# Kernel optimization log

Hardware: AMD Instinct MI355X
Metric: run time of the kernel (lower is better)

The kernel has to match this reference:

```python
import jax, jax.numpy as jnp
import numpy as np

B, T, D, H = 4, 2048, 1024, 16


def setup_inputs() -> dict:
    key = jax.random.key(0)
    ks = jax.random.split(key, 5)
    s = 0.02  # keep activations sane
    return {
        "x": jax.random.normal(ks[0], (B, T, D), jnp.float32),
        "Wq": jax.random.normal(ks[1], (D, D), jnp.float32) * s,
        "bq": jnp.zeros((D,), jnp.float32),
        "Wk": jax.random.normal(ks[2], (D, D), jnp.float32) * s,
        "bk": jnp.zeros((D,), jnp.float32),
        "Wv": jax.random.normal(ks[3], (D, D), jnp.float32) * s,
        "bv": jnp.zeros((D,), jnp.float32),
        "Wo": jax.random.normal(ks[4], (D, D), jnp.float32) * s,
        "bo": jnp.zeros((D,), jnp.float32),
    }


def _split_heads(t):  # (B,T,D) -> (B,H,T,d)
    b, s, d = t.shape
    return t.reshape(b, s, H, d // H).transpose(0, 2, 1, 3)


def reference(x, Wq, bq, Wk, bk, Wv, bv, Wo, bo):
    d_k = D // H
    q = _split_heads(x @ Wq + bq)  # (B,H,T,d)
    k = _split_heads(x @ Wk + bk)
    v = _split_heads(x @ Wv + bv)
    # scaled dot-product similarities (B,H,T,T)
    scores = jnp.einsum("bhqd,bhkd->bhqk", q, k) / jnp.sqrt(jnp.asarray(d_k, x.dtype))
    # causal mask: masked_fill(tril==0, -inf)
    causal = jnp.tril(jnp.ones((T, T), bool))
    scores = jnp.where(causal, scores, -jnp.inf)
    attn = jax.nn.softmax(scores, axis=-1)
    ctx = jnp.einsum("bhqk,bhkd->bhqd", attn, v)  # (B,H,T,d)
    ctx = ctx.transpose(0, 2, 1, 3).reshape(x.shape[0], T, D)
    return ctx @ Wo + bo
```

## Files before the change

### kernel.cpp

```cpp
#include <hip/hip_runtime.h>
#include <hip/hip_bf16.h>

typedef unsigned short u16;
typedef __attribute__((ext_vector_type(8))) short bf16x8;
typedef __attribute__((ext_vector_type(4))) short bf16x4;
typedef __attribute__((ext_vector_type(4))) float f32x4;

#define DD 1024
#define TT 2048
#define HH 16
#define BB 4
#define DK 64
#define MM 8192

#define QSCALE 0.180336880f

__device__ __forceinline__ u16 f2b(float x) {
  __hip_bfloat16 h = __float2bfloat16(x);
  return *reinterpret_cast<u16*>(&h);
}

#define GLD16(gp, lp)                                                         \
  __builtin_amdgcn_global_load_lds(                                           \
      (const __attribute__((address_space(1))) unsigned int*)(gp),            \
      (__attribute__((address_space(3))) unsigned int*)(lp), 16, 0, 0)

__global__ __launch_bounds__(256) void cast_bf16_kernel(
    const float* __restrict__ src, u16* __restrict__ dst, int n) {
  int i = (blockIdx.x * 256 + threadIdx.x) * 4;
  if (i + 3 < n) {
    float4 v = *reinterpret_cast<const float4*>(src + i);
    ushort4 o;
    o.x = f2b(v.x); o.y = f2b(v.y); o.z = f2b(v.z); o.w = f2b(v.w);
    *reinterpret_cast<ushort4*>(dst + i) = o;
  }
}

__global__ __launch_bounds__(256) void transpose_cast_kernel(
    const float* __restrict__ W0, const float* __restrict__ W1,
    const float* __restrict__ W2, const float* __restrict__ W3,
    u16* __restrict__ O0, u16* __restrict__ O1,
    u16* __restrict__ O2, u16* __restrict__ O3) {
  const float* W; u16* O;
  switch (blockIdx.z) {
    case 0: W = W0; O = O0; break;
    case 1: W = W1; O = O1; break;
    case 2: W = W2; O = O2; break;
    default: W = W3; O = O3; break;
  }
  __shared__ float tile[32][33];
  int tx = threadIdx.x, ty = threadIdx.y;
  int bx = blockIdx.x * 32;
  int by = blockIdx.y * 32;
#pragma unroll
  for (int j = 0; j < 4; j++)
    tile[ty + j * 8][tx] = W[(size_t)(by + ty + j * 8) * DD + bx + tx];
  __syncthreads();
#pragma unroll
  for (int j = 0; j < 4; j++)
    O[(size_t)(bx + ty + j * 8) * DD + by + tx] = f2b(tile[tx][ty + j * 8]);
}

__global__ __launch_bounds__(256) void gemm_qkv_kernel(
    const u16* __restrict__ A,
    const u16* __restrict__ WtQ, const u16* __restrict__ WtK,
    const u16* __restrict__ WtV,
    const float* __restrict__ bq, const float* __restrict__ bk,
    const float* __restrict__ bv,
    u16* __restrict__ Qo, u16* __restrict__ Ko, u16* __restrict__ Vo) {
  __shared__ __align__(16) u16 As[128 * 32];
  __shared__ __align__(16) u16 Bs[128 * 32];
  __shared__ __align__(16) u16 Vs[128 * 136];
  int z = blockIdx.z;
  const u16* Bt = (z == 0) ? WtQ : ((z == 1) ? WtK : WtV);
  const float* bias = (z == 0) ? bq : ((z == 1) ? bk : bv);
  int tid = threadIdx.x;
  int wave = tid >> 6, lane = tid & 63;
  int quad = lane >> 4, l16 = lane & 15;
  int m0 = blockIdx.x * 128, n0 = blockIdx.y * 128;
  int wm = (wave >> 1) * 64, wn = (wave & 1) * 64;

  f32x4 acc[4][4];
#pragma unroll
  for (int i = 0; i < 4; i++)
#pragma unroll
    for (int j = 0; j < 4; j++) acc[i][j] = (f32x4){0.f, 0.f, 0.f, 0.f};

  for (int k0 = 0; k0 < DD; k0 += 32) {
#pragma unroll
    for (int c = 0; c < 2; c++) {
      int idx = tid * 8 + c * 2048;
      int row = idx >> 5, kk = idx & 31;
      GLD16(A + (size_t)(m0 + row) * DD + k0 + kk, As + idx);
      GLD16(Bt + (size_t)(n0 + row) * DD + k0 + kk, Bs + idx);
    }
    __syncthreads();
    bf16x8 af[4], bfr[4];
#pragma unroll
    for (int mb = 0; mb < 4; mb++)
      af[mb] = *reinterpret_cast<const bf16x8*>(&As[(wm + mb * 16 + l16) * 32 + quad * 8]);
#pragma unroll
    for (int nb = 0; nb < 4; nb++)
      bfr[nb] = *reinterpret_cast<const bf16x8*>(&Bs[(wn + nb * 16 + l16) * 32 + quad * 8]);
#pragma unroll
    for (int mb = 0; mb < 4; mb++)
#pragma unroll
      for (int nb = 0; nb < 4; nb++)
        acc[mb][nb] = __builtin_amdgcn_mfma_f32_16x16x32_bf16(
            af[mb], bfr[nb], acc[mb][nb], 0, 0, 0);
    __syncthreads();
  }

  if (z == 2) {
#pragma unroll
    for (int mb = 0; mb < 4; mb++)
#pragma unroll
      for (int nb = 0; nb < 4; nb++) {
        int col = wn + nb * 16 + l16;
        float bv2 = bias[n0 + col];
#pragma unroll
        for (int r = 0; r < 4; r++) {
          int row = wm + mb * 16 + quad * 4 + r;
          Vs[col * 136 + row] = f2b(acc[mb][nb][r] + bv2);
        }
      }
    __syncthreads();
    int b = m0 >> 11;
    int tloc = m0 & 2047;
#pragma unroll
    for (int i = 0; i < 8; i++) {
      int idx = tid * 8 + i * 2048;
      int row = idx >> 7, col = idx & 127;
      uint4 v = *reinterpret_cast<const uint4*>(&Vs[row * 136 + col]);
      int ncol = n0 + row, h = ncol >> 6, dd = ncol & 63;
      *reinterpret_cast<uint4*>(
          Vo + (((size_t)(b * HH + h) * DK) + dd) * TT + tloc + col) = v;
    }
    return;
  }

  u16* outp = (z == 0) ? Qo : Ko;
  float scale = (z == 0) ? QSCALE : 1.0f;
#pragma unroll
  for (int mb = 0; mb < 4; mb++) {
#pragma unroll
    for (int nb = 0; nb < 4; nb++) {
      int col = n0 + wn + nb * 16 + l16;
      float bv2 = bias[col];
#pragma unroll
      for (int r = 0; r < 4; r++) {
        int row = m0 + wm + mb * 16 + quad * 4 + r;
        float val = (acc[mb][nb][r] + bv2) * scale;
        int hh = col >> 6, dd = col & 63;
        int b = row >> 11, t = row & 2047;
        outp[(((size_t)(b * HH + hh) * TT) + t) * DK + dd] = f2b(val);
      }
    }
  }
}

__global__ __launch_bounds__(256) void gemm_out_kernel(
    const u16* __restrict__ A, const u16* __restrict__ Bt,
    const float* __restrict__ bias, float* __restrict__ outp) {
  __shared__ __align__(16) u16 As[128 * 32];
  __shared__ __align__(16) u16 Bs[128 * 32];
  int tid = threadIdx.x;
  int wave = tid >> 6, lane = tid & 63;
  int quad = lane >> 4, l16 = lane & 15;
  int m0 = blockIdx.x * 128, n0 = blockIdx.y * 128;
  int wm = (wave >> 1) * 64, wn = (wave & 1) * 64;

  f32x4 acc[4][4];
#pragma unroll
  for (int i = 0; i < 4; i++)
#pragma unroll
    for (int j = 0; j < 4; j++) acc[i][j] = (f32x4){0.f, 0.f, 0.f, 0.f};

  for (int k0 = 0; k0 < DD; k0 += 32) {
#pragma unroll
    for (int c = 0; c < 2; c++) {
      int idx = tid * 8 + c * 2048;
      int row = idx >> 5, kk = idx & 31;
      GLD16(A + (size_t)(m0 + row) * DD + k0 + kk, As + idx);
      GLD16(Bt + (size_t)(n0 + row) * DD + k0 + kk, Bs + idx);
    }
    __syncthreads();
    bf16x8 af[4], bfr[4];
#pragma unroll
    for (int mb = 0; mb < 4; mb++)
      af[mb] = *reinterpret_cast<const bf16x8*>(&As[(wm + mb * 16 + l16) * 32 + quad * 8]);
#pragma unroll
    for (int nb = 0; nb < 4; nb++)
      bfr[nb] = *reinterpret_cast<const bf16x8*>(&Bs[(wn + nb * 16 + l16) * 32 + quad * 8]);
#pragma unroll
    for (int mb = 0; mb < 4; mb++)
#pragma unroll
      for (int nb = 0; nb < 4; nb++)
        acc[mb][nb] = __builtin_amdgcn_mfma_f32_16x16x32_bf16(
            af[mb], bfr[nb], acc[mb][nb], 0, 0, 0);
    __syncthreads();
  }

#pragma unroll
  for (int mb = 0; mb < 4; mb++) {
#pragma unroll
    for (int nb = 0; nb < 4; nb++) {
      int col = n0 + wn + nb * 16 + l16;
      float bv = bias[col];
#pragma unroll
      for (int r = 0; r < 4; r++) {
        int row = m0 + wm + mb * 16 + quad * 4 + r;
        outp[(size_t)row * DD + col] = acc[mb][nb][r] + bv;
      }
    }
  }
}

__global__ __launch_bounds__(512, 4) void attn_kernel(
    const u16* __restrict__ Q, const u16* __restrict__ K,
    const u16* __restrict__ VT, u16* __restrict__ ctx) {
  __shared__ __align__(16) u16 Ks[2][64][72];
  __shared__ __align__(16) u16 Vt[2][64][72];
  __shared__ float fbuf[8][16];

  int tid = threadIdx.x;
  int wave = tid >> 6, lane = tid & 63;
  int quad = lane >> 4, l16 = lane & 15;
  int bid = blockIdx.x;
  int bh = bid & 63;
  int px = bid >> 6;
  int b = bh >> 4, h = bh & 15;
  const u16* Qh = Q + (size_t)bh * TT * DK;
  const u16* Kh = K + (size_t)bh * TT * DK;
  const u16* Vh = VT + (size_t)bh * DK * TT;
  int sidx = tid * 8;

  for (int phase = 0; phase < 2; phase++) {
    int qt = phase ? (15 - px) : px;
    int ktmax = 2 * qt + 1;
    int dtile = 2 * qt + (wave >> 2);
    int qrl = (wave * 16 + l16) & 63;
    __syncthreads();

    const u16* qrow = Qh + (size_t)(qt * 128 + wave * 16 + l16) * DK + quad * 8;
    bf16x8 qf0 = *reinterpret_cast<const bf16x8*>(qrow);
    bf16x8 qf1 = *reinterpret_cast<const bf16x8*>(qrow + 32);

    uint4 kpre = *reinterpret_cast<const uint4*>(Kh + sidx);
    uint4 vpre = *reinterpret_cast<const uint4*>(Vh + (size_t)(sidx >> 6) * TT + (sidx & 63));
    *reinterpret_cast<uint4*>(&Ks[0][sidx >> 6][sidx & 63]) = kpre;
    *reinterpret_cast<uint4*>(&Vt[0][sidx >> 6][sidx & 63]) = vpre;
    __syncthreads();

    f32x4 oacc[4];
#pragma unroll
    for (int dt = 0; dt < 4; dt++) oacc[dt] = (f32x4){0.f, 0.f, 0.f, 0.f};
    float lsum = 0.f;

    for (int kt = 0; kt <= ktmax; kt++) {
      int cur = kt & 1, nxt = cur ^ 1;
      bool more = kt < ktmax;
      if (more) {
        kpre = *reinterpret_cast<const uint4*>(Kh + (size_t)(kt + 1) * 4096 + sidx);
        vpre = *reinterpret_cast<const uint4*>(
            Vh + (size_t)(sidx >> 6) * TT + (kt + 1) * 64 + (sidx & 63));
      }

      if (kt <= dtile) {
        f32x4 sacc[4];
#pragma unroll
        for (int kb = 0; kb < 4; kb++) sacc[kb] = (f32x4){0.f, 0.f, 0.f, 0.f};
#pragma unroll
        for (int kb = 0; kb < 4; kb++) {
          bf16x8 kf0 = *reinterpret_cast<const bf16x8*>(&Ks[cur][kb * 16 + l16][quad * 8]);
          bf16x8 kf1 = *reinterpret_cast<const bf16x8*>(&Ks[cur][kb * 16 + l16][32 + quad * 8]);
          sacc[kb] = __builtin_amdgcn_mfma_f32_16x16x32_bf16(kf0, qf0, sacc[kb], 0, 0, 0);
          sacc[kb] = __builtin_amdgcn_mfma_f32_16x16x32_bf16(kf1, qf1, sacc[kb], 0, 0, 0);
        }

        if (kt == dtile) {
#pragma unroll
          for (int kb = 0; kb < 4; kb++)
#pragma unroll
            for (int r = 0; r < 4; r++)
              if (kb * 16 + quad * 4 + r > qrl) sacc[kb][r] = -__builtin_inff();
        }

#pragma unroll
        for (int kb = 0; kb < 4; kb++) {
          float p0 = exp2f(sacc[kb][0]), p1 = exp2f(sacc[kb][1]);
          float p2 = exp2f(sacc[kb][2]), p3 = exp2f(sacc[kb][3]);
          lsum += (p0 + p1) + (p2 + p3);
          union { unsigned u[2]; bf16x4 v; } pk;
          pk.u[0] = (unsigned)f2b(p0) | ((unsigned)f2b(p1) << 16);
          pk.u[1] = (unsigned)f2b(p2) | ((unsigned)f2b(p3) << 16);
#pragma unroll
          for (int dt = 0; dt < 4; dt++) {
            bf16x4 vf = *reinterpret_cast<const bf16x4*>(
                &Vt[cur][dt * 16 + l16][kb * 16 + quad * 4]);
            oacc[dt] = __builtin_amdgcn_mfma_f32_16x16x16bf16_1k(pk.v, vf, oacc[dt], 0, 0, 0);
          }
        }
      }

      if (more) {
        *reinterpret_cast<uint4*>(&Ks[nxt][sidx >> 6][sidx & 63]) = kpre;
        *reinterpret_cast<uint4*>(&Vt[nxt][sidx >> 6][sidx & 63]) = vpre;
      }
      __syncthreads();
    }

    lsum += __shfl_xor(lsum, 16);
    lsum += __shfl_xor(lsum, 32);
    if (quad == 0) fbuf[wave][l16] = lsum;
    asm volatile("s_waitcnt lgkmcnt(0)" ::: "memory");
    f32x4 lv = *reinterpret_cast<const f32x4*>(&fbuf[wave][quad * 4]);
    f32x4 inv;
#pragma unroll
    for (int r = 0; r < 4; r++) inv[r] = 1.0f / lv[r];

    u16* Obuf = &Ks[0][0][0];
#pragma unroll
    for (int dt = 0; dt < 4; dt++)
#pragma unroll
      for (int r = 0; r < 4; r++)
        Obuf[(wave * 16 + quad * 4 + r) * 72 + dt * 16 + l16] =
            f2b(oacc[dt][r] * inv[r]);
    asm volatile("s_waitcnt lgkmcnt(0)" ::: "memory");
#pragma unroll
    for (int i = 0; i < 2; i++) {
      int idx = lane * 8 + i * 512;
      int row = idx >> 6, colc = idx & 63;
      uint4 v = *reinterpret_cast<const uint4*>(&Obuf[(wave * 16 + row) * 72 + colc]);
      int t = qt * 128 + wave * 16 + row;
      *reinterpret_cast<uint4*>(
          ctx + ((size_t)(b * TT + t)) * DD + h * DK + colc) = v;
    }
  }
}

extern "C" void kernel_launch(void* const* d_in, const int* in_sizes, int n_in,
                              void* d_out, int out_size, void* d_ws, size_t ws_size,
                              hipStream_t stream) {
  const float* x  = (const float*)d_in[0];
  const float* Wq = (const float*)d_in[1];
  const float* bq = (const float*)d_in[2];
  const float* Wk = (const float*)d_in[3];
  const float* bk = (const float*)d_in[4];
  const float* Wv = (const float*)d_in[5];
  const float* bv = (const float*)d_in[6];
  const float* Wo = (const float*)d_in[7];
  const float* bo = (const float*)d_in[8];
  float* out = (float*)d_out;

  char* ws = (char*)d_ws;
  size_t off = 0;
  u16* xb  = (u16*)(ws + off); off += (size_t)MM * DD * 2;
  u16* wtq = (u16*)(ws + off); off += (size_t)DD * DD * 2;
  u16* wtk = (u16*)(ws + off); off += (size_t)DD * DD * 2;
  u16* wtv = (u16*)(ws + off); off += (size_t)DD * DD * 2;
  u16* wto = (u16*)(ws + off); off += (size_t)DD * DD * 2;
  u16* Qb  = (u16*)(ws + off); off += (size_t)MM * DD * 2;
  u16* Kb  = (u16*)(ws + off); off += (size_t)MM * DD * 2;
  u16* VTb = (u16*)(ws + off); off += (size_t)MM * DD * 2;
  u16* ctx = (u16*)(ws + off); off += (size_t)MM * DD * 2;

  {
    int n = MM * DD;
    cast_bf16_kernel<<<n / 1024, 256, 0, stream>>>(x, xb, n);
  }
  {
    dim3 grid(DD / 32, DD / 32, 4);
    dim3 block(32, 8);
    transpose_cast_kernel<<<grid, block, 0, stream>>>(Wq, Wk, Wv, Wo, wtq, wtk, wtv, wto);
  }
  {
    dim3 grid(MM / 128, DD / 128, 3);
    gemm_qkv_kernel<<<grid, 256, 0, stream>>>(xb, wtq, wtk, wtv, bq, bk, bv,
                                              Qb, Kb, VTb);
  }
  {
    attn_kernel<<<512, 512, 0, stream>>>(Qb, Kb, VTb, ctx);
  }
  {
    dim3 grid(MM / 128, DD / 128);
    gemm_out_kernel<<<grid, 256, 0, stream>>>(ctx, wto, bo, out);
  }
}
```

Measured before the change: 271.8 us.

## Enlarge attention query tile to 256 rows and write transposed V directly

The attention kernel now runs 1024-thread blocks that each handle 256 query rows instead of 128. This halves the number of times K/V tiles are streamed into shared memory per head, at the cost of smaller per-thread loads and fewer, larger blocks. The V projection epilogue swaps the MFMA operand order so the accumulators come out already transposed, and writes them straight to global memory. That removes the LDS staging buffer and one barrier, but the global stores become 2-byte scattered writes instead of 16-byte vector stores.

```diff
diff --git a/kernel.cpp b/kernel.cpp
--- a/kernel.cpp
+++ b/kernel.cpp
@@ -70,7 +70,6 @@
     u16* __restrict__ Qo, u16* __restrict__ Ko, u16* __restrict__ Vo) {
   __shared__ __align__(16) u16 As[128 * 32];
   __shared__ __align__(16) u16 Bs[128 * 32];
-  __shared__ __align__(16) u16 Vs[128 * 136];
   int z = blockIdx.z;
   const u16* Bt = (z == 0) ? WtQ : ((z == 1) ? WtK : WtV);
   const float* bias = (z == 0) ? bq : ((z == 1) ? bk : bv);
@@ -102,40 +101,41 @@
 #pragma unroll
     for (int nb = 0; nb < 4; nb++)
       bfr[nb] = *reinterpret_cast<const bf16x8*>(&Bs[(wn + nb * 16 + l16) * 32 + quad * 8]);
-#pragma unroll
-    for (int mb = 0; mb < 4; mb++)
-#pragma unroll
-      for (int nb = 0; nb < 4; nb++)
-        acc[mb][nb] = __builtin_amdgcn_mfma_f32_16x16x32_bf16(
-            af[mb], bfr[nb], acc[mb][nb], 0, 0, 0);
+    if (z != 2) {
+#pragma unroll
+      for (int mb = 0; mb < 4; mb++)
+#pragma unroll
+        for (int nb = 0; nb < 4; nb++)
+          acc[mb][nb] = __builtin_amdgcn_mfma_f32_16x16x32_bf16(
+              af[mb], bfr[nb], acc[mb][nb], 0, 0, 0);
+    } else {
+#pragma unroll
+      for (int mb = 0; mb < 4; mb++)
+#pragma unroll
+        for (int nb = 0; nb < 4; nb++)
+          acc[mb][nb] = __builtin_amdgcn_mfma_f32_16x16x32_bf16(
+              bfr[nb], af[mb], acc[mb][nb], 0, 0, 0);
+    }
     __syncthreads();
   }
 
   if (z == 2) {
-#pragma unroll
-    for (int mb = 0; mb < 4; mb++)
-#pragma unroll
-      for (int nb = 0; nb < 4; nb++) {
-        int col = wn + nb * 16 + l16;
-        float bv2 = bias[n0 + col];
-#pragma unroll
-        for (int r = 0; r < 4; r++) {
-          int row = wm + mb * 16 + quad * 4 + r;
-          Vs[col * 136 + row] = f2b(acc[mb][nb][r] + bv2);
+    int b = m0 >> 11;
+    int tbase = (m0 & 2047) + wm;
+#pragma unroll
+    for (int nb = 0; nb < 4; nb++)
+#pragma unroll
+      for (int r = 0; r < 4; r++) {
+        int ncol = n0 + wn + nb * 16 + quad * 4 + r;
+        int h = ncol >> 6, dd = ncol & 63;
+        float bv2 = bias[ncol];
+        u16* basep = Vo + (((size_t)(b * HH + h) * DK) + dd) * TT;
+#pragma unroll
+        for (int mb = 0; mb < 4; mb++) {
+          int t = tbase + mb * 16 + l16;
+          basep[t] = f2b(acc[mb][nb][r] + bv2);
         }
       }
-    __syncthreads();
-    int b = m0 >> 11;
-    int tloc = m0 & 2047;
-#pragma unroll
-    for (int i = 0; i < 8; i++) {
-      int idx = tid * 8 + i * 2048;
-      int row = idx >> 7, col = idx & 127;
-      uint4 v = *reinterpret_cast<const uint4*>(&Vs[row * 136 + col]);
-      int ncol = n0 + row, h = ncol >> 6, dd = ncol & 63;
-      *reinterpret_cast<uint4*>(
-          Vo + (((size_t)(b * HH + h) * DK) + dd) * TT + tloc + col) = v;
-    }
     return;
   }
 
@@ -216,12 +216,11 @@
   }
 }
 
-__global__ __launch_bounds__(512, 4) void attn_kernel(
+__global__ __launch_bounds__(1024, 4) void attn_kernel(
     const u16* __restrict__ Q, const u16* __restrict__ K,
     const u16* __restrict__ VT, u16* __restrict__ ctx) {
-  __shared__ __align__(16) u16 Ks[2][64][72];
-  __shared__ __align__(16) u16 Vt[2][64][72];
-  __shared__ float fbuf[8][16];
+  __shared__ __align__(16) u16 smem[4][64][72];
+  __shared__ float fbuf[16][16];
 
   int tid = threadIdx.x;
   int wave = tid >> 6, lane = tid & 63;
@@ -233,23 +232,24 @@
   const u16* Qh = Q + (size_t)bh * TT * DK;
   const u16* Kh = K + (size_t)bh * TT * DK;
   const u16* Vh = VT + (size_t)bh * DK * TT;
-  int sidx = tid * 8;
+  int sidx = tid * 4;
+  int srow = sidx >> 6, scol = sidx & 63;
 
   for (int phase = 0; phase < 2; phase++) {
-    int qt = phase ? (15 - px) : px;
-    int ktmax = 2 * qt + 1;
-    int dtile = 2 * qt + (wave >> 2);
+    int qt = phase ? (7 - px) : px;
+    int ktmax = 4 * qt + 3;
+    int dtile = 4 * qt + (wave >> 2);
     int qrl = (wave * 16 + l16) & 63;
     __syncthreads();
 
-    const u16* qrow = Qh + (size_t)(qt * 128 + wave * 16 + l16) * DK + quad * 8;
+    const u16* qrow = Qh + (size_t)(qt * 256 + wave * 16 + l16) * DK + quad * 8;
     bf16x8 qf0 = *reinterpret_cast<const bf16x8*>(qrow);
     bf16x8 qf1 = *reinterpret_cast<const bf16x8*>(qrow + 32);
 
-    uint4 kpre = *reinterpret_cast<const uint4*>(Kh + sidx);
-    uint4 vpre = *reinterpret_cast<const uint4*>(Vh + (size_t)(sidx >> 6) * TT + (sidx & 63));
-    *reinterpret_cast<uint4*>(&Ks[0][sidx >> 6][sidx & 63]) = kpre;
-    *reinterpret_cast<uint4*>(&Vt[0][sidx >> 6][sidx & 63]) = vpre;
+    uint2 kpre = *reinterpret_cast<const uint2*>(Kh + sidx);
+    uint2 vpre = *reinterpret_cast<const uint2*>(Vh + (size_t)srow * TT + scol);
+    *reinterpret_cast<uint2*>(&smem[0][srow][scol]) = kpre;
+    *reinterpret_cast<uint2*>(&smem[2][srow][scol]) = vpre;
     __syncthreads();
 
     f32x4 oacc[4];
@@ -261,9 +261,9 @@
       int cur = kt & 1, nxt = cur ^ 1;
       bool more = kt < ktmax;
       if (more) {
-        kpre = *reinterpret_cast<const uint4*>(Kh + (size_t)(kt + 1) * 4096 + sidx);
-        vpre = *reinterpret_cast<const uint4*>(
-            Vh + (size_t)(sidx >> 6) * TT + (kt + 1) * 64 + (sidx & 63));
+        kpre = *reinterpret_cast<const uint2*>(Kh + (size_t)(kt + 1) * 4096 + sidx);
+        vpre = *reinterpret_cast<const uint2*>(
+            Vh + (size_t)srow * TT + (kt + 1) * 64 + scol);
       }
 
       if (kt <= dtile) {
@@ -272,8 +272,8 @@
         for (int kb = 0; kb < 4; kb++) sacc[kb] = (f32x4){0.f, 0.f, 0.f, 0.f};
 #pragma unroll
         for (int kb = 0; kb < 4; kb++) {
-          bf16x8 kf0 = *reinterpret_cast<const bf16x8*>(&Ks[cur][kb * 16 + l16][quad * 8]);
-          bf16x8 kf1 = *reinterpret_cast<const bf16x8*>(&Ks[cur][kb * 16 + l16][32 + quad * 8]);
+          bf16x8 kf0 = *reinterpret_cast<const bf16x8*>(&smem[cur][kb * 16 + l16][quad * 8]);
+          bf16x8 kf1 = *reinterpret_cast<const bf16x8*>(&smem[cur][kb * 16 + l16][32 + quad * 8]);
           sacc[kb] = __builtin_amdgcn_mfma_f32_16x16x32_bf16(kf0, qf0, sacc[kb], 0, 0, 0);
           sacc[kb] = __builtin_amdgcn_mfma_f32_16x16x32_bf16(kf1, qf1, sacc[kb], 0, 0, 0);
         }
@@ -297,15 +297,15 @@
 #pragma unroll
           for (int dt = 0; dt < 4; dt++) {
             bf16x4 vf = *reinterpret_cast<const bf16x4*>(
-                &Vt[cur][dt * 16 + l16][kb * 16 + quad * 4]);
+                &smem[2 + cur][dt * 16 + l16][kb * 16 + quad * 4]);
             oacc[dt] = __builtin_amdgcn_mfma_f32_16x16x16bf16_1k(pk.v, vf, oacc[dt], 0, 0, 0);
           }
         }
       }
 
       if (more) {
-        *reinterpret_cast<uint4*>(&Ks[nxt][sidx >> 6][sidx & 63]) = kpre;
-        *reinterpret_cast<uint4*>(&Vt[nxt][sidx >> 6][sidx & 63]) = vpre;
+        *reinterpret_cast<uint2*>(&smem[nxt][srow][scol]) = kpre;
+        *reinterpret_cast<uint2*>(&smem[2 + nxt][srow][scol]) = vpre;
       }
       __syncthreads();
     }
@@ -319,7 +319,7 @@
 #pragma unroll
     for (int r = 0; r < 4; r++) inv[r] = 1.0f / lv[r];
 
-    u16* Obuf = &Ks[0][0][0];
+    u16* Obuf = &smem[0][0][0];
 #pragma unroll
     for (int dt = 0; dt < 4; dt++)
 #pragma unroll
@@ -332,7 +332,7 @@
       int idx = lane * 8 + i * 512;
       int row = idx >> 6, colc = idx & 63;
       uint4 v = *reinterpret_cast<const uint4*>(&Obuf[(wave * 16 + row) * 72 + colc]);
-      int t = qt * 128 + wave * 16 + row;
+      int t = qt * 256 + wave * 16 + row;
       *reinterpret_cast<uint4*>(
           ctx + ((size_t)(b * TT + t)) * DD + h * DK + colc) = v;
     }
@@ -380,7 +380,7 @@
                                               Qb, Kb, VTb);
   }
   {
-    attn_kernel<<<512, 512, 0, stream>>>(Qb, Kb, VTb, ctx);
+    attn_kernel<<<256, 1024, 0, stream>>>(Qb, Kb, VTb, ctx);
   }
   {
     dim3 grid(MM / 128, DD / 128);
```

Result: no change. 275.4 us (+1.3%).
